# Kernel optimization log

Hardware: AMD Instinct MI355X
Metric: run time of the kernel (lower is better)

The kernel has to match this reference:

```python
import jax, jax.numpy as jnp
import numpy as np

EPS = 1e-5


def conv1x1(x, w, b=None):
    # x: [B,C,H,W], w: [O,C] (1x1 conv kernel squeezed)
    y = jnp.einsum('bchw,oc->bohw', x, w)
    if b is not None:
        y = y + b[None, :, None, None]
    return y


def bn_inf(x, g, b, m, v):
    scale = g / jnp.sqrt(v + EPS)
    return (x - m[None, :, None, None]) * scale[None, :, None, None] + b[None, :, None, None]


def setup_inputs() -> dict:
    B, C, H, W = 2, 256, 80, 80
    Ck, Cv, Co = 64, 128, 256
    key = jax.random.key(0)
    ks = jax.random.split(key, 16)
    d = {}
    d['x'] = jax.random.normal(ks[0], (B, C, H, W), dtype=jnp.float32)
    d['y'] = jax.random.normal(ks[1], (B, C, H, W), dtype=jnp.float32)
    s = 1.0 / np.sqrt(C)
    d['fk_w'] = jax.random.normal(ks[2], (Ck, C), dtype=jnp.float32) * s
    d['fk_g'] = jnp.ones((Ck,), jnp.float32)
    d['fk_b'] = jnp.zeros((Ck,), jnp.float32)
    d['fk_m'] = jax.random.normal(ks[3], (Ck,), dtype=jnp.float32) * 0.1
    d['fk_v'] = jax.random.uniform(ks[4], (Ck,), minval=0.5, maxval=1.5, dtype=jnp.float32)
    d['fq_w'] = jax.random.normal(ks[5], (Ck, C), dtype=jnp.float32) * s
    d['fq_g'] = jnp.ones((Ck,), jnp.float32)
    d['fq_b'] = jnp.zeros((Ck,), jnp.float32)
    d['fq_m'] = jax.random.normal(ks[6], (Ck,), dtype=jnp.float32) * 0.1
    d['fq_v'] = jax.random.uniform(ks[7], (Ck,), minval=0.5, maxval=1.5, dtype=jnp.float32)
    d['fv_w'] = jax.random.normal(ks[8], (Cv, C), dtype=jnp.float32) * s
    d['fv_b'] = jnp.zeros((Cv,), jnp.float32)
    d['W_w'] = jax.random.normal(ks[9], (Co, Cv), dtype=jnp.float32) * (1.0 / np.sqrt(Cv))
    d['W_b'] = jnp.zeros((Co,), jnp.float32)
    d['gamma'] = jnp.array([0.5], jnp.float32)
    return d


def reference(x, y, fk_w, fk_g, fk_b, fk_m, fk_v, fq_w, fq_g, fq_b, fq_m, fq_v, fv_w, fv_b, W_w, W_b, gamma):
    B, C, H, W = x.shape
    Ck = fk_w.shape[0]
    Cv = fv_w.shape[0]
    N = H * W
    # key from x, query/value from y (1x1 conv + BN projections)
    k = bn_inf(conv1x1(x, fk_w), fk_g, fk_b, fk_m, fk_v).reshape(B, Ck, N)          # [B,Ck,N]
    q = bn_inf(conv1x1(y, fq_w), fq_g, fq_b, fq_m, fq_v).reshape(B, Ck, N)          # [B,Ck,N]
    v = conv1x1(y, fv_w, fv_b).reshape(B, Cv, N)                                     # [B,Cv,N]
    sim = jnp.einsum('bkn,bkm->bnm', q, k) * (Ck ** -0.5)                            # [B,N,N]
    sim = jax.nn.softmax(sim, axis=-1)
    ctx = jnp.einsum('bnm,bvm->bvn', sim, v).reshape(B, Cv, H, W)                    # [B,Cv,H,W]
    ctx = conv1x1(ctx, W_w, W_b)                                                     # [B,Co,H,W]
    return gamma[0] * ctx + x
```

## Files before the change

kernel.cpp:

```cpp
#include <hip/hip_runtime.h>
#include <math.h>

#define NB   2
#define CIN  256
#define NN   6400
#define CKd  64
#define CVd  128
#define COd  256

using bf16   = __bf16;
using bf16x4 = __attribute__((ext_vector_type(4))) bf16;
using bf16x8 = __attribute__((ext_vector_type(8))) bf16;
using f32x4  = __attribute__((ext_vector_type(4))) float;

__device__ __forceinline__ void lds_cp16(const void* g, void* l) {
    __builtin_amdgcn_global_load_lds((const __attribute__((address_space(1))) void*)g,
                                     (__attribute__((address_space(3))) void*)l, 16, 0, 0);
}

__global__ void prep_kernel(const float* __restrict__ fk_w, const float* __restrict__ fk_g,
                            const float* __restrict__ fk_b, const float* __restrict__ fk_m,
                            const float* __restrict__ fk_v,
                            const float* __restrict__ fq_w, const float* __restrict__ fq_g,
                            const float* __restrict__ fq_b, const float* __restrict__ fq_m,
                            const float* __restrict__ fq_v,
                            const float* __restrict__ fv_w, const float* __restrict__ fv_b,
                            const float* __restrict__ W_w,  const float* __restrict__ W_b,
                            bf16* __restrict__ wkb, bf16* __restrict__ wqb,
                            bf16* __restrict__ wvb, bf16* __restrict__ wob,
                            float* __restrict__ bias)
{
    const int idx = blockIdx.x * 256 + threadIdx.x;
    const float QS = 0.18033688011112042f;
    if (idx < 16384) {
        const int co = idx >> 8;
        const float a = fk_g[co] * rsqrtf(fk_v[co] + 1e-5f);
        wkb[idx] = (bf16)(fk_w[idx] * a);
    } else if (idx < 32768) {
        const int i = idx - 16384, co = i >> 8;
        const float a = fq_g[co] * rsqrtf(fq_v[co] + 1e-5f) * QS;
        wqb[i] = (bf16)(fq_w[i] * a);
    } else if (idx < 65536) {
        const int i = idx - 32768;
        wvb[i] = (bf16)fv_w[i];
    } else if (idx < 98304) {
        const int i = idx - 65536;
        wob[i] = (bf16)W_w[i];
    } else if (idx < 98816) {
        const int j = idx - 98304;
        if (j < 64)       { const float a = fk_g[j] * rsqrtf(fk_v[j] + 1e-5f); bias[j] = fk_b[j] - fk_m[j] * a; }
        else if (j < 128) { const int c = j - 64; const float a = fq_g[c] * rsqrtf(fq_v[c] + 1e-5f); bias[j] = (fq_b[c] - fq_m[c] * a) * QS; }
        else if (j < 256) bias[j] = fv_b[j - 128];
        else              bias[j] = W_b[j - 256];
    }
}

__launch_bounds__(256, 2)
__global__ void projkqv_kernel(const float* __restrict__ x, const float* __restrict__ y,
                               const bf16* __restrict__ wkb, const bf16* __restrict__ wqb,
                               const bf16* __restrict__ wvb, const float* __restrict__ bias,
                               bf16* __restrict__ kb, bf16* __restrict__ qb, bf16* __restrict__ vb)
{
    __shared__ __align__(16) bf16 sbuf[64 * 256];
    __shared__ __align__(16) bf16 wbuf[64 * 256];

    const int tid  = threadIdx.x;
    const int lane = tid & 63, wav = tid >> 6;
    const int l15  = lane & 15, quad = lane >> 4;
    const int b    = blockIdx.z, m = blockIdx.y;
    const int n0   = blockIdx.x * 64;

    const float* srcg = ((m == 0) ? x : y) + (size_t)b * CIN * NN;
    const bf16* wg    = (m == 0) ? wkb : (m == 1) ? wqb : (wvb + (size_t)(m - 2) * 64 * CIN);

    {
        const int r2  = lane >> 5;
        const int c32 = lane & 31;
#pragma unroll
        for (int i = 0; i < 8; ++i) {
            const int rg = wav * 16 + i * 2;
            const int r  = rg + r2;
            const int cs = c32 ^ (r & 7);
            lds_cp16(wg + (size_t)r * 256 + cs * 8, &wbuf[rg * 256]);
        }
    }

    {
        const int nl = (tid & 15) * 4;
        const int cq = tid >> 4;
#pragma unroll
        for (int g = 0; g < 2; ++g) {
            const int cb = (cq + g * 16) * 8;
            float4 v[8];
#pragma unroll
            for (int e = 0; e < 8; ++e)
                v[e] = *(const float4*)(srcg + (size_t)(cb + e) * NN + n0 + nl);
#pragma unroll
            for (int i = 0; i < 4; ++i) {
                const int n = nl + i;
                bf16x8 pk;
#pragma unroll
                for (int e = 0; e < 8; ++e) pk[e] = (bf16)(&v[e].x)[i];
                *(bf16x8*)&sbuf[n * 256 + (((cb >> 3) ^ (n & 7)) * 8)] = pk;
            }
        }
    }
    __syncthreads();

    const int key = l15 & 7;
    f32x4 acc[4];
#pragma unroll
    for (int j = 0; j < 4; ++j) acc[j] = (f32x4){0.f, 0.f, 0.f, 0.f};

    if (m < 2) {
        const int arow = wav * 16 + l15;
#pragma unroll
        for (int k4 = 0; k4 < 32; k4 += 4) {
            const bf16x8 af = *(const bf16x8*)&sbuf[arow * 256 + ((k4 + quad) ^ key) * 8];
#pragma unroll
            for (int nt = 0; nt < 4; ++nt) {
                const int brow = nt * 16 + l15;
                const bf16x8 bfw = *(const bf16x8*)&wbuf[brow * 256 + ((k4 + quad) ^ key) * 8];
                acc[nt] = __builtin_amdgcn_mfma_f32_16x16x32_bf16(af, bfw, acc[nt], 0, 0, 0);
            }
        }
        const float* bs = bias + m * 64;
        bf16* dst = (m == 0) ? kb : qb;
        const int nb = n0 + wav * 16;
#pragma unroll
        for (int nt = 0; nt < 4; ++nt) {
            const float bv = bs[nt * 16 + l15];
#pragma unroll
            for (int r = 0; r < 4; ++r) {
                const int n = nb + quad * 4 + r;
                dst[((size_t)b * NN + n) * CKd + nt * 16 + l15] = (bf16)(acc[nt][r] + bv);
            }
        }
    } else {
        const int arow = wav * 16 + l15;
#pragma unroll
        for (int k4 = 0; k4 < 32; k4 += 4) {
            const bf16x8 af = *(const bf16x8*)&wbuf[arow * 256 + ((k4 + quad) ^ key) * 8];
#pragma unroll
            for (int nt = 0; nt < 4; ++nt) {
                const int brow = nt * 16 + l15;
                const bf16x8 bfy = *(const bf16x8*)&sbuf[brow * 256 + ((k4 + quad) ^ key) * 8];
                acc[nt] = __builtin_amdgcn_mfma_f32_16x16x32_bf16(af, bfy, acc[nt], 0, 0, 0);
            }
        }
        const int cv0 = (m - 2) * 64 + wav * 16;
#pragma unroll
        for (int r = 0; r < 4; ++r) {
            const int cv = cv0 + quad * 4 + r;
            const float bv = bias[128 + cv];
#pragma unroll
            for (int nt = 0; nt < 4; ++nt)
                vb[((size_t)b * CVd + cv) * NN + n0 + nt * 16 + l15] = (bf16)(acc[nt][r] + bv);
        }
    }
}

__launch_bounds__(256, 2)
__global__ void attn_kernel(const bf16* __restrict__ qb, const bf16* __restrict__ kb,
                            const bf16* __restrict__ vb,
                            bf16* __restrict__ pO, float* __restrict__ pl, int KS)
{
    __shared__ __align__(16) bf16 kbuf[2][64 * 64];
    __shared__ __align__(16) bf16 vbuf[2][128 * 64];
    __shared__ __align__(16) bf16 p_lds[4][2][16][64];

    const int lane = threadIdx.x & 63;
    const int wav  = threadIdx.x >> 6;
    const int l15  = lane & 15;
    const int quad = lane >> 4;
    const int r8   = lane >> 3;
    const int c_src = (lane & 7) ^ r8;
    const int sw   = l15 & 7;
    const int pkey = (l15 & 7) << 1;

    const int id    = blockIdx.x;
    const int ks    = id % KS;
    const int rst   = id / KS;
    const int b     = rst & 1;
    const int qtile = rst >> 1;
    const int q0    = qtile * 256 + wav * 64;

    const bf16* qrow = qb + (size_t)b * NN * CKd;
    const bf16* krow = kb + (size_t)b * NN * CKd;
    const bf16* vrow = vb + (size_t)b * CVd * NN;

    bf16x8 qf[4][2];
#pragma unroll
    for (int qt = 0; qt < 4; ++qt)
#pragma unroll
        for (int s = 0; s < 2; ++s)
            qf[qt][s] = *(const bf16x8*)(qrow + (size_t)(q0 + qt * 16 + l15) * CKd + s * 32 + quad * 8);

    f32x4 acc[4][8];
#pragma unroll
    for (int qt = 0; qt < 4; ++qt)
#pragma unroll
        for (int cv = 0; cv < 8; ++cv) acc[qt][cv] = (f32x4){0.f, 0.f, 0.f, 0.f};
    float psum[4] = {0.f, 0.f, 0.f, 0.f};

    const int t0 = (100 * ks) / KS;
    const int nt = (100 * (ks + 1)) / KS - t0;

    auto stage = [&](int t, int bi) {
        const int key0 = t * 64;
        lds_cp16(krow + (size_t)(key0 + wav * 8 + r8) * CKd + c_src * 8,
                 &kbuf[bi][(wav * 8) * 64]);
        lds_cp16(krow + (size_t)(key0 + (wav + 4) * 8 + r8) * CKd + c_src * 8,
                 &kbuf[bi][((wav + 4) * 8) * 64]);
#pragma unroll
        for (int g4 = 0; g4 < 4; ++g4) {
            const int g = wav * 4 + g4;
            lds_cp16(vrow + (size_t)(g * 8 + r8) * NN + key0 + c_src * 8,
                     &vbuf[bi][(g * 8) * 64]);
        }
    };

    stage(t0, 0);

    for (int t = 0; t < nt; ++t) {
        __syncthreads();
        if (t + 1 < nt) stage(t0 + t + 1, (t + 1) & 1);
        const bf16* kcur = &kbuf[t & 1][0];
        const bf16* vcur = &vbuf[t & 1][0];

#pragma unroll
        for (int ph = 0; ph < 2; ++ph) {
            f32x4 s4[2][4];
#pragma unroll
            for (int kt = 0; kt < 4; ++kt) {
                const int rr = kt * 16 + l15;
                const bf16x8 kf0 = *(const bf16x8*)&kcur[rr * 64 + ((quad ^ sw) * 8)];
                const bf16x8 kf1 = *(const bf16x8*)&kcur[rr * 64 + (((4 + quad) ^ sw) * 8)];
#pragma unroll
                for (int qtl = 0; qtl < 2; ++qtl) {
                    const int qt = ph * 2 + qtl;
                    f32x4 z = (f32x4){0.f, 0.f, 0.f, 0.f};
                    z = __builtin_amdgcn_mfma_f32_16x16x32_bf16(kf0, qf[qt][0], z, 0, 0, 0);
                    z = __builtin_amdgcn_mfma_f32_16x16x32_bf16(kf1, qf[qt][1], z, 0, 0, 0);
                    s4[qtl][kt] = z;
                }
            }

#pragma unroll
            for (int qtl = 0; qtl < 2; ++qtl) {
                float ps = 0.f;
#pragma unroll
                for (int kt = 0; kt < 4; ++kt) {
                    bf16x4 pk;
#pragma unroll
                    for (int r = 0; r < 4; ++r) {
                        const float p = exp2f(s4[qtl][kt][r] - 11.541560327111707f);
                        ps += p;
                        pk[r] = (bf16)p;
                    }
                    *(bf16x4*)&p_lds[wav][qtl][l15][((kt * 4 + quad) ^ pkey) * 4] = pk;
                }
                psum[ph * 2 + qtl] += ps;
            }

#pragma unroll
            for (int sp = 0; sp < 2; ++sp) {
                const bf16x8 pf0 = *(const bf16x8*)&p_lds[wav][0][l15][((sp * 8 + quad * 2) ^ pkey) * 4];
                const bf16x8 pf1 = *(const bf16x8*)&p_lds[wav][1][l15][((sp * 8 + quad * 2) ^ pkey) * 4];
#pragma unroll
                for (int cvt = 0; cvt < 8; ++cvt) {
                    const int rr = cvt * 16 + l15;
                    const bf16x8 vf = *(const bf16x8*)&vcur[rr * 64 + (((sp * 4 + quad) ^ sw) * 8)];
                    acc[ph * 2 + 0][cvt] = __builtin_amdgcn_mfma_f32_16x16x32_bf16(vf, pf0, acc[ph * 2 + 0][cvt], 0, 0, 0);
                    acc[ph * 2 + 1][cvt] = __builtin_amdgcn_mfma_f32_16x16x32_bf16(vf, pf1, acc[ph * 2 + 1][cvt], 0, 0, 0);
                }
            }
        }
    }

    __syncthreads();
    bf16* tbuf = &p_lds[wav][0][0][0];
    const size_t pb = (size_t)ks * NB + b;
#pragma unroll
    for (int qt = 0; qt < 4; ++qt) {
        psum[qt] += __shfl_xor(psum[qt], 16);
        psum[qt] += __shfl_xor(psum[qt], 32);
#pragma unroll
        for (int cvt = 0; cvt < 8; ++cvt) {
            bf16x4 pk;
#pragma unroll
            for (int r = 0; r < 4; ++r) pk[r] = (bf16)acc[qt][cvt][r];
            const int u = (cvt * 4 + quad) ^ (l15 << 1);
            *(bf16x4*)&tbuf[l15 * 128 + u * 4] = pk;
        }
#pragma unroll
        for (int j = 0; j < 4; ++j) {
            const int row = j * 4 + (lane >> 4);
            const int g   = ((lane & 15) * 2) ^ ((row & 15) << 1);
            const bf16x8 vv = *(const bf16x8*)&tbuf[row * 128 + g * 4];
            *(bf16x8*)(pO + (pb * NN + q0 + qt * 16) * CVd + j * 512 + lane * 8) = vv;
        }
        if (quad == 0) pl[pb * NN + q0 + qt * 16 + l15] = psum[qt];
    }
}

__launch_bounds__(256, 2)
__global__ void outproj_kernel(const bf16* __restrict__ pO, const float* __restrict__ pl,
                               const bf16* __restrict__ wob, const float* __restrict__ bias,
                               const float* __restrict__ x, const float* __restrict__ gam,
                               float* __restrict__ out, int KS)
{
    __shared__ __align__(16) bf16 wbuf[256 * 128];
    __shared__ __align__(16) bf16 cbuf[32 * 128];
    __shared__ float Lrow[32];

    const int tid  = threadIdx.x;
    const int lane = tid & 63, wav = tid >> 6;
    const int l15  = lane & 15, quad = lane >> 4;
    const int b    = blockIdx.y;
    const int n0   = blockIdx.x * 32;

    {
        const int r4 = lane >> 4;
        const int c  = lane & 15;
#pragma unroll
        for (int i = 0; i < 16; ++i) {
            const int rg = wav * 64 + i * 4;
            const int r  = rg + r4;
            const int cs = c ^ (r & 7);
            lds_cp16(wob + (size_t)r * CVd + cs * 8, &wbuf[rg * 128]);
        }
    }

    const int tn = tid >> 3;
    const int tc = (tid & 7) * 16;
    float vacc[16];
#pragma unroll
    for (int i = 0; i < 16; ++i) vacc[i] = 0.f;
    for (int ksi = 0; ksi < KS; ++ksi) {
        const bf16* src = pO + ((size_t)(ksi * NB + b) * NN + n0 + tn) * CVd + tc;
#pragma unroll
        for (int j = 0; j < 2; ++j) {
            const bf16x8 v = *(const bf16x8*)(src + j * 8);
#pragma unroll
            for (int e = 0; e < 8; ++e) vacc[j * 8 + e] += (float)v[e];
        }
    }
    if (tid < 32) {
        float L = 0.f;
        for (int ksi = 0; ksi < KS; ++ksi)
            L += pl[(size_t)(ksi * NB + b) * NN + n0 + tid];
        Lrow[tid] = 1.0f / L;
    }
    __syncthreads();
    {
        const float rL = Lrow[tn];
#pragma unroll
        for (int j = 0; j < 2; ++j) {
            bf16x8 o;
#pragma unroll
            for (int e = 0; e < 8; ++e) o[e] = (bf16)(vacc[j * 8 + e] * rL);
            const int c = (tid & 7) * 2 + j;
            *(bf16x8*)&cbuf[tn * 128 + ((c ^ (tn & 7)) * 8)] = o;
        }
    }
    __syncthreads();

    f32x4 acc[4][2];
#pragma unroll
    for (int i = 0; i < 4; ++i)
#pragma unroll
        for (int j = 0; j < 2; ++j) acc[i][j] = (f32x4){0.f, 0.f, 0.f, 0.f};

#pragma unroll
    for (int kk = 0; kk < 4; ++kk) {
#pragma unroll
        for (int cot = 0; cot < 4; ++cot) {
            const int arow = wav * 64 + cot * 16 + l15;
            const bf16x8 af = *(const bf16x8*)&wbuf[arow * 128 + (((kk * 4 + quad) ^ (arow & 7)) * 8)];
#pragma unroll
            for (int nt = 0; nt < 2; ++nt) {
                const int brow = nt * 16 + l15;
                const bf16x8 bfc = *(const bf16x8*)&cbuf[brow * 128 + (((kk * 4 + quad) ^ (brow & 7)) * 8)];
                acc[cot][nt] = __builtin_amdgcn_mfma_f32_16x16x32_bf16(af, bfc, acc[cot][nt], 0, 0, 0);
            }
        }
    }

    const float gm = gam[0];
#pragma unroll
    for (int cot = 0; cot < 4; ++cot) {
#pragma unroll
        for (int r = 0; r < 4; ++r) {
            const int co = wav * 64 + cot * 16 + quad * 4 + r;
            const float bv = bias[256 + co];
#pragma unroll
            for (int nt = 0; nt < 2; ++nt) {
                const int n = n0 + nt * 16 + l15;
                const size_t a = ((size_t)b * COd + co) * NN + n;
                out[a] = gm * (acc[cot][nt][r] + bv) + x[a];
            }
        }
    }
}

extern "C" void kernel_launch(void* const* d_in, const int* in_sizes, int n_in,
                              void* d_out, int out_size, void* d_ws, size_t ws_size,
                              hipStream_t stream)
{
    const float* x     = (const float*)d_in[0];
    const float* y     = (const float*)d_in[1];
    const float* fk_w  = (const float*)d_in[2];
    const float* fk_g  = (const float*)d_in[3];
    const float* fk_b  = (const float*)d_in[4];
    const float* fk_m  = (const float*)d_in[5];
    const float* fk_v  = (const float*)d_in[6];
    const float* fq_w  = (const float*)d_in[7];
    const float* fq_g  = (const float*)d_in[8];
    const float* fq_b  = (const float*)d_in[9];
    const float* fq_m  = (const float*)d_in[10];
    const float* fq_v  = (const float*)d_in[11];
    const float* fv_w  = (const float*)d_in[12];
    const float* fv_b  = (const float*)d_in[13];
    const float* W_w   = (const float*)d_in[14];
    const float* W_b   = (const float*)d_in[15];
    const float* gamma = (const float*)d_in[16];
    float* out = (float*)d_out;

    char* ws = (char*)d_ws;
    size_t off = 0;
    auto carve = [&](size_t bytes) -> char* {
        char* p = ws + off;
        off = (off + bytes + 255) & ~(size_t)255;
        return p;
    };

    bf16*  kb   = (bf16*)carve((size_t)NB * NN * CKd * 2);
    bf16*  qbuf = (bf16*)carve((size_t)NB * NN * CKd * 2);
    bf16*  vb   = (bf16*)carve((size_t)NB * CVd * NN * 2);
    bf16*  wkb  = (bf16*)carve((size_t)CKd * CIN * 2);
    bf16*  wqb  = (bf16*)carve((size_t)CKd * CIN * 2);
    bf16*  wvb  = (bf16*)carve((size_t)CVd * CIN * 2);
    bf16*  wob  = (bf16*)carve((size_t)COd * CVd * 2);
    float* bias = (float*)carve(512 * 4);

    const size_t region = ws_size - off;
    const size_t per_ks = (size_t)NB * NN * CVd * 2 + (size_t)NB * NN * 4 + 512;
    int KS = 1;
    {
        const int cand[6] = {10, 8, 5, 4, 2, 1};
        for (int i = 0; i < 6; ++i)
            if ((size_t)cand[i] * per_ks <= region) { KS = cand[i]; break; }
    }
    bf16*  pO = (bf16*)carve((size_t)KS * NB * NN * CVd * 2);
    float* pl = (float*)carve((size_t)KS * NB * NN * 4);

    const dim3 blk(256);
    prep_kernel<<<386, blk, 0, stream>>>(fk_w, fk_g, fk_b, fk_m, fk_v,
                                         fq_w, fq_g, fq_b, fq_m, fq_v,
                                         fv_w, fv_b, W_w, W_b,
                                         wkb, wqb, wvb, wob, bias);
    projkqv_kernel<<<dim3(100, 4, NB), blk, 0, stream>>>(x, y, wkb, wqb, wvb, bias, kb, qbuf, vb);
    attn_kernel<<<dim3(25 * NB * KS), blk, 0, stream>>>(qbuf, kb, vb, pO, pl, KS);
    outproj_kernel<<<dim3(200, NB), blk, 0, stream>>>(pO, pl, wob, bias, x, gamma, out, KS);
}
```

Baseline: 172.9 us.

## Halve LDS in projection/outproj, fold softmax offset into MFMA init, overlap attn phases

The projection kernel now stages the 256-wide reduction in two 128-wide passes, halving its LDS so launch bounds can rise to 4 blocks per CU. The output projection splits its 256 output channels into two passes with half-sized weight LDS, prefetches the next split's partials, and computes the per-row normaliser per thread instead of through shared memory. The attention kernel seeds the score accumulator with the softmax offset constant so the subtraction drops out. It also software-pipelines the second query-half's exp/P write with the first half's PV MFMAs using a double-buffered P tile and s_setprio hints. The costs are an extra barrier per pass, more LDS in attention, and more register pressure under the tighter occupancy targets.

```diff
diff --git a/kernel.cpp b/kernel.cpp
--- a/kernel.cpp
+++ b/kernel.cpp
@@ -55,14 +55,14 @@
     }
 }
 
-__launch_bounds__(256, 2)
+__launch_bounds__(256, 4)
 __global__ void projkqv_kernel(const float* __restrict__ x, const float* __restrict__ y,
                                const bf16* __restrict__ wkb, const bf16* __restrict__ wqb,
                                const bf16* __restrict__ wvb, const float* __restrict__ bias,
                                bf16* __restrict__ kb, bf16* __restrict__ qb, bf16* __restrict__ vb)
 {
-    __shared__ __align__(16) bf16 sbuf[64 * 256];
-    __shared__ __align__(16) bf16 wbuf[64 * 256];
+    __shared__ __align__(16) bf16 sbuf[64 * 128];
+    __shared__ __align__(16) bf16 wbuf[64 * 128];
 
     const int tid  = threadIdx.x;
     const int lane = tid & 63, wav = tid >> 6;
@@ -73,24 +73,29 @@
     const float* srcg = ((m == 0) ? x : y) + (size_t)b * CIN * NN;
     const bf16* wg    = (m == 0) ? wkb : (m == 1) ? wqb : (wvb + (size_t)(m - 2) * 64 * CIN);
 
-    {
-        const int r2  = lane >> 5;
-        const int c32 = lane & 31;
-#pragma unroll
-        for (int i = 0; i < 8; ++i) {
-            const int rg = wav * 16 + i * 2;
-            const int r  = rg + r2;
-            const int cs = c32 ^ (r & 7);
-            lds_cp16(wg + (size_t)r * 256 + cs * 8, &wbuf[rg * 256]);
-        }
-    }
-
-    {
-        const int nl = (tid & 15) * 4;
-        const int cq = tid >> 4;
-#pragma unroll
-        for (int g = 0; g < 2; ++g) {
-            const int cb = (cq + g * 16) * 8;
+    const int key = l15 & 7;
+    f32x4 acc[4];
+#pragma unroll
+    for (int j = 0; j < 4; ++j) acc[j] = (f32x4){0.f, 0.f, 0.f, 0.f};
+
+    for (int p = 0; p < 2; ++p) {
+        if (p) __syncthreads();
+
+        {
+            const int r4  = lane >> 4;
+            const int c16 = lane & 15;
+#pragma unroll
+            for (int i = 0; i < 4; ++i) {
+                const int rg = wav * 16 + i * 4;
+                const int r  = rg + r4;
+                const int cs = c16 ^ (r & 7);
+                lds_cp16(wg + (size_t)r * 256 + p * 128 + cs * 8, &wbuf[rg * 128]);
+            }
+        }
+        {
+            const int nl = (tid & 15) * 4;
+            const int cq = tid >> 4;
+            const int cb = p * 128 + cq * 8;
             float4 v[8];
 #pragma unroll
             for (int e = 0; e < 8; ++e)
@@ -101,29 +106,39 @@
                 bf16x8 pk;
 #pragma unroll
                 for (int e = 0; e < 8; ++e) pk[e] = (bf16)(&v[e].x)[i];
-                *(bf16x8*)&sbuf[n * 256 + (((cb >> 3) ^ (n & 7)) * 8)] = pk;
-            }
-        }
-    }
-    __syncthreads();
-
-    const int key = l15 & 7;
-    f32x4 acc[4];
-#pragma unroll
-    for (int j = 0; j < 4; ++j) acc[j] = (f32x4){0.f, 0.f, 0.f, 0.f};
+                *(bf16x8*)&sbuf[n * 128 + ((cq ^ (n & 7)) * 8)] = pk;
+            }
+        }
+        __syncthreads();
+
+        if (m < 2) {
+            const int arow = wav * 16 + l15;
+#pragma unroll
+            for (int k4 = 0; k4 < 16; k4 += 4) {
+                const bf16x8 af = *(const bf16x8*)&sbuf[arow * 128 + (((k4 + quad) ^ key) * 8)];
+#pragma unroll
+                for (int nt = 0; nt < 4; ++nt) {
+                    const int brow = nt * 16 + l15;
+                    const bf16x8 bfw = *(const bf16x8*)&wbuf[brow * 128 + (((k4 + quad) ^ key) * 8)];
+                    acc[nt] = __builtin_amdgcn_mfma_f32_16x16x32_bf16(af, bfw, acc[nt], 0, 0, 0);
+                }
+            }
+        } else {
+            const int arow = wav * 16 + l15;
+#pragma unroll
+            for (int k4 = 0; k4 < 16; k4 += 4) {
+                const bf16x8 af = *(const bf16x8*)&wbuf[arow * 128 + (((k4 + quad) ^ key) * 8)];
+#pragma unroll
+                for (int nt = 0; nt < 4; ++nt) {
+                    const int brow = nt * 16 + l15;
+                    const bf16x8 bfy = *(const bf16x8*)&sbuf[brow * 128 + (((k4 + quad) ^ key) * 8)];
+                    acc[nt] = __builtin_amdgcn_mfma_f32_16x16x32_bf16(af, bfy, acc[nt], 0, 0, 0);
+                }
+            }
+        }
+    }
 
     if (m < 2) {
-        const int arow = wav * 16 + l15;
-#pragma unroll
-        for (int k4 = 0; k4 < 32; k4 += 4) {
-            const bf16x8 af = *(const bf16x8*)&sbuf[arow * 256 + ((k4 + quad) ^ key) * 8];
-#pragma unroll
-            for (int nt = 0; nt < 4; ++nt) {
-                const int brow = nt * 16 + l15;
-                const bf16x8 bfw = *(const bf16x8*)&wbuf[brow * 256 + ((k4 + quad) ^ key) * 8];
-                acc[nt] = __builtin_amdgcn_mfma_f32_16x16x32_bf16(af, bfw, acc[nt], 0, 0, 0);
-            }
-        }
         const float* bs = bias + m * 64;
         bf16* dst = (m == 0) ? kb : qb;
         const int nb = n0 + wav * 16;
@@ -137,17 +152,6 @@
             }
         }
     } else {
-        const int arow = wav * 16 + l15;
-#pragma unroll
-        for (int k4 = 0; k4 < 32; k4 += 4) {
-            const bf16x8 af = *(const bf16x8*)&wbuf[arow * 256 + ((k4 + quad) ^ key) * 8];
-#pragma unroll
-            for (int nt = 0; nt < 4; ++nt) {
-                const int brow = nt * 16 + l15;
-                const bf16x8 bfy = *(const bf16x8*)&sbuf[brow * 256 + ((k4 + quad) ^ key) * 8];
-                acc[nt] = __builtin_amdgcn_mfma_f32_16x16x32_bf16(af, bfy, acc[nt], 0, 0, 0);
-            }
-        }
         const int cv0 = (m - 2) * 64 + wav * 16;
 #pragma unroll
         for (int r = 0; r < 4; ++r) {
@@ -167,7 +171,7 @@
 {
     __shared__ __align__(16) bf16 kbuf[2][64 * 64];
     __shared__ __align__(16) bf16 vbuf[2][128 * 64];
-    __shared__ __align__(16) bf16 p_lds[4][2][16][64];
+    __shared__ __align__(16) bf16 p_lds[4][2][2][16][64];
 
     const int lane = threadIdx.x & 63;
     const int wav  = threadIdx.x >> 6;
@@ -196,6 +200,9 @@
         for (int s = 0; s < 2; ++s)
             qf[qt][s] = *(const bf16x8*)(qrow + (size_t)(q0 + qt * 16 + l15) * CKd + s * 32 + quad * 8);
 
+    const float ZC = -11.541560327111707f;
+    const f32x4 zini = (f32x4){ZC, ZC, ZC, ZC};
+
     f32x4 acc[4][8];
 #pragma unroll
     for (int qt = 0; qt < 4; ++qt)
@@ -228,58 +235,108 @@
         const bf16* kcur = &kbuf[t & 1][0];
         const bf16* vcur = &vbuf[t & 1][0];
 
-#pragma unroll
-        for (int ph = 0; ph < 2; ++ph) {
-            f32x4 s4[2][4];
+        f32x4 s4[2][4];
+
+        __builtin_amdgcn_s_setprio(1);
+#pragma unroll
+        for (int kt = 0; kt < 4; ++kt) {
+            const int rr = kt * 16 + l15;
+            const bf16x8 kf0 = *(const bf16x8*)&kcur[rr * 64 + ((quad ^ sw) * 8)];
+            const bf16x8 kf1 = *(const bf16x8*)&kcur[rr * 64 + (((4 + quad) ^ sw) * 8)];
+#pragma unroll
+            for (int qtl = 0; qtl < 2; ++qtl) {
+                f32x4 z = zini;
+                z = __builtin_amdgcn_mfma_f32_16x16x32_bf16(kf0, qf[qtl][0], z, 0, 0, 0);
+                z = __builtin_amdgcn_mfma_f32_16x16x32_bf16(kf1, qf[qtl][1], z, 0, 0, 0);
+                s4[qtl][kt] = z;
+            }
+        }
+        __builtin_amdgcn_s_setprio(0);
+
+#pragma unroll
+        for (int qtl = 0; qtl < 2; ++qtl) {
+            float ps = 0.f;
 #pragma unroll
             for (int kt = 0; kt < 4; ++kt) {
-                const int rr = kt * 16 + l15;
-                const bf16x8 kf0 = *(const bf16x8*)&kcur[rr * 64 + ((quad ^ sw) * 8)];
-                const bf16x8 kf1 = *(const bf16x8*)&kcur[rr * 64 + (((4 + quad) ^ sw) * 8)];
-#pragma unroll
-                for (int qtl = 0; qtl < 2; ++qtl) {
-                    const int qt = ph * 2 + qtl;
-                    f32x4 z = (f32x4){0.f, 0.f, 0.f, 0.f};
-                    z = __builtin_amdgcn_mfma_f32_16x16x32_bf16(kf0, qf[qt][0], z, 0, 0, 0);
-                    z = __builtin_amdgcn_mfma_f32_16x16x32_bf16(kf1, qf[qt][1], z, 0, 0, 0);
-                    s4[qtl][kt] = z;
-                }
-            }
-
+                bf16x4 pk;
+#pragma unroll
+                for (int r = 0; r < 4; ++r) {
+                    const float p = exp2f(s4[qtl][kt][r]);
+                    ps += p;
+                    pk[r] = (bf16)p;
+                }
+                *(bf16x4*)&p_lds[wav][0][qtl][l15][((kt * 4 + quad) ^ pkey) * 4] = pk;
+            }
+            psum[qtl] += ps;
+        }
+
+        __builtin_amdgcn_s_setprio(1);
+#pragma unroll
+        for (int kt = 0; kt < 4; ++kt) {
+            const int rr = kt * 16 + l15;
+            const bf16x8 kf0 = *(const bf16x8*)&kcur[rr * 64 + ((quad ^ sw) * 8)];
+            const bf16x8 kf1 = *(const bf16x8*)&kcur[rr * 64 + (((4 + quad) ^ sw) * 8)];
 #pragma unroll
             for (int qtl = 0; qtl < 2; ++qtl) {
-                float ps = 0.f;
-#pragma unroll
-                for (int kt = 0; kt < 4; ++kt) {
+                f32x4 z = zini;
+                z = __builtin_amdgcn_mfma_f32_16x16x32_bf16(kf0, qf[2 + qtl][0], z, 0, 0, 0);
+                z = __builtin_amdgcn_mfma_f32_16x16x32_bf16(kf1, qf[2 + qtl][1], z, 0, 0, 0);
+                s4[qtl][kt] = z;
+            }
+        }
+        __builtin_amdgcn_s_setprio(0);
+
+        {
+            bf16x8 pfA, pfB;
+#pragma unroll
+            for (int u = 0; u < 8; ++u) {
+                const int sp = u >> 2;
+                if ((u & 3) == 0) {
+                    pfA = *(const bf16x8*)&p_lds[wav][0][0][l15][((sp * 8 + quad * 2) ^ pkey) * 4];
+                    pfB = *(const bf16x8*)&p_lds[wav][0][1][l15][((sp * 8 + quad * 2) ^ pkey) * 4];
+                }
+                {
+                    const int qtl = u >> 2, kt = u & 3;
                     bf16x4 pk;
+                    float ps = 0.f;
 #pragma unroll
                     for (int r = 0; r < 4; ++r) {
-                        const float p = exp2f(s4[qtl][kt][r] - 11.541560327111707f);
+                        const float p = exp2f(s4[qtl][kt][r]);
                         ps += p;
                         pk[r] = (bf16)p;
                     }
-                    *(bf16x4*)&p_lds[wav][qtl][l15][((kt * 4 + quad) ^ pkey) * 4] = pk;
-                }
-                psum[ph * 2 + qtl] += ps;
-            }
-
-#pragma unroll
-            for (int sp = 0; sp < 2; ++sp) {
-                const bf16x8 pf0 = *(const bf16x8*)&p_lds[wav][0][l15][((sp * 8 + quad * 2) ^ pkey) * 4];
-                const bf16x8 pf1 = *(const bf16x8*)&p_lds[wav][1][l15][((sp * 8 + quad * 2) ^ pkey) * 4];
-#pragma unroll
-                for (int cvt = 0; cvt < 8; ++cvt) {
+                    *(bf16x4*)&p_lds[wav][1][qtl][l15][((kt * 4 + quad) ^ pkey) * 4] = pk;
+                    psum[2 + qtl] += ps;
+                }
+#pragma unroll
+                for (int v2 = 0; v2 < 2; ++v2) {
+                    const int cvt = (u & 3) * 2 + v2;
                     const int rr = cvt * 16 + l15;
                     const bf16x8 vf = *(const bf16x8*)&vcur[rr * 64 + (((sp * 4 + quad) ^ sw) * 8)];
-                    acc[ph * 2 + 0][cvt] = __builtin_amdgcn_mfma_f32_16x16x32_bf16(vf, pf0, acc[ph * 2 + 0][cvt], 0, 0, 0);
-                    acc[ph * 2 + 1][cvt] = __builtin_amdgcn_mfma_f32_16x16x32_bf16(vf, pf1, acc[ph * 2 + 1][cvt], 0, 0, 0);
-                }
-            }
-        }
+                    acc[0][cvt] = __builtin_amdgcn_mfma_f32_16x16x32_bf16(vf, pfA, acc[0][cvt], 0, 0, 0);
+                    acc[1][cvt] = __builtin_amdgcn_mfma_f32_16x16x32_bf16(vf, pfB, acc[1][cvt], 0, 0, 0);
+                }
+            }
+        }
+
+        __builtin_amdgcn_s_setprio(1);
+#pragma unroll
+        for (int sp = 0; sp < 2; ++sp) {
+            const bf16x8 pf0 = *(const bf16x8*)&p_lds[wav][1][0][l15][((sp * 8 + quad * 2) ^ pkey) * 4];
+            const bf16x8 pf1 = *(const bf16x8*)&p_lds[wav][1][1][l15][((sp * 8 + quad * 2) ^ pkey) * 4];
+#pragma unroll
+            for (int cvt = 0; cvt < 8; ++cvt) {
+                const int rr = cvt * 16 + l15;
+                const bf16x8 vf = *(const bf16x8*)&vcur[rr * 64 + (((sp * 4 + quad) ^ sw) * 8)];
+                acc[2][cvt] = __builtin_amdgcn_mfma_f32_16x16x32_bf16(vf, pf0, acc[2][cvt], 0, 0, 0);
+                acc[3][cvt] = __builtin_amdgcn_mfma_f32_16x16x32_bf16(vf, pf1, acc[3][cvt], 0, 0, 0);
+            }
+        }
+        __builtin_amdgcn_s_setprio(0);
     }
 
     __syncthreads();
-    bf16* tbuf = &p_lds[wav][0][0][0];
+    bf16* tbuf = &p_lds[wav][0][0][0][0];
     const size_t pb = (size_t)ks * NB + b;
 #pragma unroll
     for (int qt = 0; qt < 4; ++qt) {
@@ -304,15 +361,14 @@
     }
 }
 
-__launch_bounds__(256, 2)
+__launch_bounds__(256, 4)
 __global__ void outproj_kernel(const bf16* __restrict__ pO, const float* __restrict__ pl,
                                const bf16* __restrict__ wob, const float* __restrict__ bias,
                                const float* __restrict__ x, const float* __restrict__ gam,
                                float* __restrict__ out, int KS)
 {
-    __shared__ __align__(16) bf16 wbuf[256 * 128];
+    __shared__ __align__(16) bf16 wbuf[128 * 128];
     __shared__ __align__(16) bf16 cbuf[32 * 128];
-    __shared__ float Lrow[32];
 
     const int tid  = threadIdx.x;
     const int lane = tid & 63, wav = tid >> 6;
@@ -320,41 +376,46 @@
     const int b    = blockIdx.y;
     const int n0   = blockIdx.x * 32;
 
-    {
+    auto stage_w = [&](int p) {
         const int r4 = lane >> 4;
         const int c  = lane & 15;
 #pragma unroll
-        for (int i = 0; i < 16; ++i) {
-            const int rg = wav * 64 + i * 4;
+        for (int i = 0; i < 8; ++i) {
+            const int rg = wav * 32 + i * 4;
             const int r  = rg + r4;
             const int cs = c ^ (r & 7);
-            lds_cp16(wob + (size_t)r * CVd + cs * 8, &wbuf[rg * 128]);
-        }
-    }
+            lds_cp16(wob + (size_t)(p * 128 + r) * CVd + cs * 8, &wbuf[rg * 128]);
+        }
+    };
+    stage_w(0);
 
     const int tn = tid >> 3;
     const int tc = (tid & 7) * 16;
+    const size_t kstr = (size_t)NB * NN * CVd;
+    const bf16* src0 = pO + ((size_t)b * NN + n0 + tn) * CVd + tc;
     float vacc[16];
 #pragma unroll
     for (int i = 0; i < 16; ++i) vacc[i] = 0.f;
+    float L = 0.f;
+
+    bf16x8 c0 = *(const bf16x8*)(src0);
+    bf16x8 c1 = *(const bf16x8*)(src0 + 8);
     for (int ksi = 0; ksi < KS; ++ksi) {
-        const bf16* src = pO + ((size_t)(ksi * NB + b) * NN + n0 + tn) * CVd + tc;
-#pragma unroll
-        for (int j = 0; j < 2; ++j) {
-            const bf16x8 v = *(const bf16x8*)(src + j * 8);
-#pragma unroll
-            for (int e = 0; e < 8; ++e) vacc[j * 8 + e] += (float)v[e];
-        }
-    }
-    if (tid < 32) {
-        float L = 0.f;
-        for (int ksi = 0; ksi < KS; ++ksi)
-            L += pl[(size_t)(ksi * NB + b) * NN + n0 + tid];
-        Lrow[tid] = 1.0f / L;
-    }
-    __syncthreads();
+        bf16x8 nx0 = c0, nx1 = c1;
+        if (ksi + 1 < KS) {
+            const bf16* s = src0 + (size_t)(ksi + 1) * kstr;
+            nx0 = *(const bf16x8*)(s);
+            nx1 = *(const bf16x8*)(s + 8);
+        }
+        L += pl[(size_t)(ksi * NB + b) * NN + n0 + tn];
+#pragma unroll
+        for (int e = 0; e < 8; ++e) vacc[e]     += (float)c0[e];
+#pragma unroll
+        for (int e = 0; e < 8; ++e) vacc[8 + e] += (float)c1[e];
+        c0 = nx0; c1 = nx1;
+    }
     {
-        const float rL = Lrow[tn];
+        const float rL = 1.0f / L;
 #pragma unroll
         for (int j = 0; j < 2; ++j) {
             bf16x8 o;
@@ -366,42 +427,53 @@
     }
     __syncthreads();
 
-    f32x4 acc[4][2];
-#pragma unroll
-    for (int i = 0; i < 4; ++i)
-#pragma unroll
-        for (int j = 0; j < 2; ++j) acc[i][j] = (f32x4){0.f, 0.f, 0.f, 0.f};
-
-#pragma unroll
-    for (int kk = 0; kk < 4; ++kk) {
-#pragma unroll
-        for (int cot = 0; cot < 4; ++cot) {
-            const int arow = wav * 64 + cot * 16 + l15;
-            const bf16x8 af = *(const bf16x8*)&wbuf[arow * 128 + (((kk * 4 + quad) ^ (arow & 7)) * 8)];
-#pragma unroll
-            for (int nt = 0; nt < 2; ++nt) {
-                const int brow = nt * 16 + l15;
-                const bf16x8 bfc = *(const bf16x8*)&cbuf[brow * 128 + (((kk * 4 + quad) ^ (brow & 7)) * 8)];
-                acc[cot][nt] = __builtin_amdgcn_mfma_f32_16x16x32_bf16(af, bfc, acc[cot][nt], 0, 0, 0);
-            }
-        }
-    }
-
     const float gm = gam[0];
-#pragma unroll
-    for (int cot = 0; cot < 4; ++cot) {
-#pragma unroll
-        for (int r = 0; r < 4; ++r) {
-            const int co = wav * 64 + cot * 16 + quad * 4 + r;
-            const float bv = bias[256 + co];
-#pragma unroll
-            for (int nt = 0; nt < 2; ++nt) {
-                const int n = n0 + nt * 16 + l15;
-                const size_t a = ((size_t)b * COd + co) * NN + n;
-                out[a] = gm * (acc[cot][nt][r] + bv) + x[a];
-            }
-        }
-    }
+
+    auto mfma_pass = [&](f32x4 (&acc)[2][2]) {
+#pragma unroll
+        for (int i = 0; i < 2; ++i)
+#pragma unroll
+            for (int j = 0; j < 2; ++j) acc[i][j] = (f32x4){0.f, 0.f, 0.f, 0.f};
+#pragma unroll
+        for (int kk = 0; kk < 4; ++kk) {
+#pragma unroll
+            for (int cot = 0; cot < 2; ++cot) {
+                const int arow = wav * 32 + cot * 16 + l15;
+                const bf16x8 af = *(const bf16x8*)&wbuf[arow * 128 + (((kk * 4 + quad) ^ (arow & 7)) * 8)];
+#pragma unroll
+                for (int nt = 0; nt < 2; ++nt) {
+                    const int brow = nt * 16 + l15;
+                    const bf16x8 bfc = *(const bf16x8*)&cbuf[brow * 128 + (((kk * 4 + quad) ^ (brow & 7)) * 8)];
+                    acc[cot][nt] = __builtin_amdgcn_mfma_f32_16x16x32_bf16(af, bfc, acc[cot][nt], 0, 0, 0);
+                }
+            }
+        }
+    };
+    auto store_pass = [&](const f32x4 (&acc)[2][2], int p) {
+#pragma unroll
+        for (int cot = 0; cot < 2; ++cot)
+#pragma unroll
+            for (int r = 0; r < 4; ++r) {
+                const int co = p * 128 + wav * 32 + cot * 16 + quad * 4 + r;
+                const float bv = bias[256 + co];
+#pragma unroll
+                for (int nt = 0; nt < 2; ++nt) {
+                    const int n = n0 + nt * 16 + l15;
+                    const size_t a = ((size_t)b * COd + co) * NN + n;
+                    out[a] = gm * (acc[cot][nt][r] + bv) + x[a];
+                }
+            }
+    };
+
+    f32x4 acc0[2][2];
+    mfma_pass(acc0);
+    __syncthreads();
+    stage_w(1);
+    store_pass(acc0, 0);
+    __syncthreads();
+    f32x4 acc1[2][2];
+    mfma_pass(acc1);
+    store_pass(acc1, 1);
 }
 
 extern "C" void kernel_launch(void* const* d_in, const int* in_sizes, int n_in,
```

Result: no change. 172.6 us (-0.2%).
